# Optimization experiments

Hardware: AMD Instinct MI355X
Metric: run time of the kernel (lower is better)

Reference implementation:

```python
import jax, jax.numpy as jnp
import numpy as np

N_NODES = 100000
N_EDGES = 600000
NFEAT = 128
HIDDEN = 64
NCLASS = 40


def _sage_conv(x, edge_index, Wl, bl, Wr):
    """PyG SAGEConv with mean aggregation.

    out = lin_l(mean_{j in N(i)} x_j) + lin_r(x_i)
    edge_index[0] = source j, edge_index[1] = target i.
    """
    src, dst = edge_index[0], edge_index[1]
    n = x.shape[0]
    # scatter-mean: sum messages then divide by in-degree (0-degree -> 0)
    msg_sum = jax.ops.segment_sum(x[src], dst, num_segments=n)          # [N, F]
    deg = jax.ops.segment_sum(jnp.ones_like(src, dtype=x.dtype), dst,
                              num_segments=n)                            # [N]
    agg = msg_sum / jnp.maximum(deg, 1.0)[:, None]
    return agg @ Wl + bl + x @ Wr


def setup_inputs() -> dict:
    key = jax.random.key(0)
    ks = jax.random.split(key, 8)
    x = jax.random.normal(ks[0], (N_NODES, NFEAT), dtype=jnp.float32)
    edge_index = jax.random.randint(ks[1], (2, N_EDGES), 0, N_NODES, dtype=jnp.int64)
    s1 = 1.0 / np.sqrt(NFEAT)
    s2 = 1.0 / np.sqrt(HIDDEN)
    return {
        "x": x,
        "edge_index": edge_index,
        "W1l": jax.random.uniform(ks[2], (NFEAT, HIDDEN), jnp.float32, -s1, s1),
        "b1": jnp.zeros((HIDDEN,), jnp.float32),
        "W1r": jax.random.uniform(ks[3], (NFEAT, HIDDEN), jnp.float32, -s1, s1),
        "W2l": jax.random.uniform(ks[4], (HIDDEN, NCLASS), jnp.float32, -s2, s2),
        "b2": jnp.zeros((NCLASS,), jnp.float32),
        "W2r": jax.random.uniform(ks[5], (HIDDEN, NCLASS), jnp.float32, -s2, s2),
    }


def reference(x, edge_index, W1l, b1, W1r, W2l, b2, W2r):
    h = _sage_conv(x, edge_index, W1l, b1, W1r)   # [N, 64]
    h = jax.nn.sigmoid(h)
    out = _sage_conv(h, edge_index, W2l, b2, W2r)  # [N, nclass]
    return out
```

## Files before the change

### kernel.cpp

```cpp
#include <hip/hip_runtime.h>
#include <hip/hip_bf16.h>


#define N_FEAT 128
#define HID 64
#define NCLS 40
#define NE_BLK 2048
#define ECAP 1536

typedef short short8 __attribute__((ext_vector_type(8)));
typedef float floatx4 __attribute__((ext_vector_type(4)));

static __device__ __forceinline__ short f2bf(float x) {
    __hip_bfloat16 h = __float2bfloat16(x);
    return __builtin_bit_cast(short, h);
}
static __device__ __forceinline__ float bf2f(unsigned short u) {
    unsigned int v = ((unsigned int)u) << 16;
    return __builtin_bit_cast(float, v);
}
static __device__ __forceinline__ void acc8(float* a, uint4 v, float w) {
    a[0] = fmaf(w, bf2f((unsigned short)(v.x & 0xffffu)), a[0]);
    a[1] = fmaf(w, bf2f((unsigned short)(v.x >> 16)), a[1]);
    a[2] = fmaf(w, bf2f((unsigned short)(v.y & 0xffffu)), a[2]);
    a[3] = fmaf(w, bf2f((unsigned short)(v.y >> 16)), a[3]);
    a[4] = fmaf(w, bf2f((unsigned short)(v.z & 0xffffu)), a[4]);
    a[5] = fmaf(w, bf2f((unsigned short)(v.z >> 16)), a[5]);
    a[6] = fmaf(w, bf2f((unsigned short)(v.w & 0xffffu)), a[6]);
    a[7] = fmaf(w, bf2f((unsigned short)(v.w >> 16)), a[7]);
}

__global__ void prep_hist(const float* __restrict__ W1l, const float* __restrict__ W1r,
                          const float* __restrict__ W2l, const float* __restrict__ W2r,
                          unsigned short* __restrict__ wt1,
                          unsigned short* __restrict__ wt2,
                          int* __restrict__ flags,
                          const int* __restrict__ ei, int ne, int n,
                          int* __restrict__ bh, int nbe) {
    __shared__ int bins[512];
    const int b = blockIdx.x, t = threadIdx.x;
    const int nbuck = (n + 255) >> 8;
    for (int i = t; i < nbuck; i += 256) bins[i] = 0;
    __syncthreads();
    const int e0 = b * NE_BLK;
    const int lim = (e0 + NE_BLK < ne) ? (e0 + NE_BLK) : ne;
    for (int e = e0 + t; e < lim; e += 256)
        atomicAdd(&bins[ei[ne + e] >> 8], 1);

    int i = b * 256 + t;
    if (i < 128 * 128) {
        int nn = i >> 7, k = i & 127;
        float v = (nn < 64) ? W1l[k * 64 + nn] : W1r[k * 64 + (nn - 64)];
        wt1[nn * 128 + k] = (unsigned short)f2bf(v);
    } else if (i < 128 * 128 + 48 * 128) {
        int j = i - 128 * 128;
        int nn = j >> 7, k = j & 127;
        float v = 0.f;
        if (nn < 40)
            v = (k < 64) ? W2l[k * 40 + nn] : W2r[(k - 64) * 40 + nn];
        wt2[nn * 128 + k] = (unsigned short)f2bf(v);
    }
    if (i < 256) flags[i] = 0;

    __syncthreads();
    for (int j = t; j < nbuck; j += 256) bh[j * nbe + b] = bins[j];
}

__global__ void scan_fused(const int* __restrict__ in, int* __restrict__ pre,
                           int m, int* __restrict__ bsums,
                           int* __restrict__ flags) {
    __shared__ int lds[256];
    __shared__ int look[128];
    __shared__ int sprefix;
    const int b = blockIdx.x, t = threadIdx.x;
    const int base = b * 2048 + t * 8;
    int v[8], s = 0;
#pragma unroll
    for (int i = 0; i < 8; ++i) {
        int idx = base + i;
        v[i] = (idx < m) ? in[idx] : 0;
        s += v[i];
    }
    lds[t] = s;
    __syncthreads();
    for (int o = 1; o < 256; o <<= 1) {
        int y = (t >= o) ? lds[t - o] : 0;
        __syncthreads();
        lds[t] += y;
        __syncthreads();
    }
    if (t == 255) {
        __hip_atomic_store(&bsums[b], lds[255], __ATOMIC_RELEASE,
                           __HIP_MEMORY_SCOPE_AGENT);
        __hip_atomic_store(&flags[b], 1, __ATOMIC_RELEASE,
                           __HIP_MEMORY_SCOPE_AGENT);
    }
    if (t < 128) look[t] = 0;
    __syncthreads();
    if (t < b) {
        while (__hip_atomic_load(&flags[t], __ATOMIC_ACQUIRE,
                                 __HIP_MEMORY_SCOPE_AGENT) == 0) {}
        look[t] = __hip_atomic_load(&bsums[t], __ATOMIC_RELAXED,
                                    __HIP_MEMORY_SCOPE_AGENT);
    }
    __syncthreads();
    if (t == 0) {
        int p = 0;
        for (int i = 0; i < b; ++i) p += look[i];
        sprefix = p;
    }
    __syncthreads();
    int run = ((t == 0) ? 0 : lds[t - 1]) + sprefix;
#pragma unroll
    for (int i = 0; i < 8; ++i) {
        run += v[i];
        int idx = base + i;
        if (idx < m) pre[idx + 1] = run;
    }
    if (b == 0 && t == 0) pre[0] = 0;
}

static __device__ __forceinline__ void gemm1_body(
    short* __restrict__ smem, const float* __restrict__ x,
    const unsigned short* __restrict__ Wt, unsigned short* __restrict__ Zl,
    unsigned short* __restrict__ Zr, int n, int bid) {
    constexpr int K = 128, LDA = K + 8, M = 128, MT = 8, KS = 4, QROW = 16;
    short* At = smem;
    short* Bt = smem + 64 * LDA;
    const int t = threadIdx.x;
    const int nodeBase = bid * 64;

    for (int q = t; q < 64 * QROW; q += 256) {
        int row = q / QROW;
        int k0 = (q % QROW) * 8;
        int node = nodeBase + row;
        short8 s = {0, 0, 0, 0, 0, 0, 0, 0};
        if (node < n) {
            const float* A = x + (size_t)node * K + k0;
            float4 v0 = *(const float4*)A;
            float4 v1 = *(const float4*)(A + 4);
            s[0] = f2bf(v0.x); s[1] = f2bf(v0.y);
            s[2] = f2bf(v0.z); s[3] = f2bf(v0.w);
            s[4] = f2bf(v1.x); s[5] = f2bf(v1.y);
            s[6] = f2bf(v1.z); s[7] = f2bf(v1.w);
        }
        *(short8*)&At[row * LDA + k0] = s;
    }
    for (int q = t; q < M * QROW; q += 256) {
        int row = q / QROW;
        int k0 = (q % QROW) * 8;
        *(short8*)&Bt[row * LDA + k0] =
            *(const short8*)((const short*)Wt + (size_t)row * K + k0);
    }
    __syncthreads();

    const int wave = t >> 6;
    const int lane = t & 63;
    const int m0 = wave * 16;
    const int fl = lane & 15;
    const int quad = lane >> 4;

    floatx4 acc[MT];
#pragma unroll
    for (int nt = 0; nt < MT; ++nt) acc[nt] = (floatx4){0.f, 0.f, 0.f, 0.f};

#pragma unroll
    for (int ks = 0; ks < KS; ++ks) {
        const int kb = ks * 32 + quad * 8;
        short8 a = *(const short8*)&At[(m0 + fl) * LDA + kb];
#pragma unroll
        for (int nt = 0; nt < MT; ++nt) {
            short8 b = *(const short8*)&Bt[(nt * 16 + fl) * LDA + kb];
            acc[nt] = __builtin_amdgcn_mfma_f32_16x16x32_bf16(a, b, acc[nt], 0, 0, 0);
        }
    }

#pragma unroll
    for (int nt = 0; nt < MT; ++nt) {
        const int col = nt * 16 + fl;
#pragma unroll
        for (int r = 0; r < 4; ++r) {
            int node = nodeBase + m0 + quad * 4 + r;
            if (node < n) {
                unsigned short v = (unsigned short)f2bf(acc[nt][r]);
                if (col < HID)
                    Zl[(size_t)node * HID + col] = v;
                else
                    Zr[(size_t)node * HID + (col - HID)] = v;
            }
        }
    }
}

__global__ __launch_bounds__(256) void scatter_gemm1(
    const int* __restrict__ ei, int ne, int n, const int* __restrict__ sbase,
    int* __restrict__ ebuf, int nbe, const float* __restrict__ x,
    const unsigned short* __restrict__ wt1, unsigned short* __restrict__ zl,
    unsigned short* __restrict__ zr) {
    __shared__ __align__(16) short smem[(64 + 128) * 136];
    const int b = blockIdx.x;
    if (b < nbe) {
        int* bins = (int*)smem;
        const int t = threadIdx.x;
        const int nbuck = (n + 255) >> 8;
        for (int i = t; i < nbuck; i += 256) bins[i] = 0;
        __syncthreads();
        const int e0 = b * NE_BLK;
        const int lim = (e0 + NE_BLK < ne) ? (e0 + NE_BLK) : ne;
        for (int e = e0 + t; e < lim; e += 256) {
            int d = ei[ne + e];
            int s = ei[e];
            int bk = d >> 8;
            int r = atomicAdd(&bins[bk], 1);
            int p = sbase[bk * nbe + b] + r;
            ebuf[p] = (int)(((unsigned)(d & 255) << 24) | (unsigned)s);
        }
    } else {
        gemm1_body(smem, x, wt1, zl, zr, n, b - nbe);
    }
}

__global__ void bucket_build(const int* __restrict__ ebuf,
                             const int* __restrict__ sbase, int nbe, int n,
                             int ne, int* __restrict__ off,
                             int* __restrict__ csr) {
    __shared__ int cnt[256];
    __shared__ int sc[256];
    __shared__ int pos[256];
    const int b = blockIdx.x;
    const int t = threadIdx.x;
    const int nbuck = (n + 255) >> 8;
    const int s0 = sbase[b * nbe];
    const int s1 = (b + 1 < nbuck) ? sbase[(b + 1) * nbe] : ne;
    cnt[t] = 0;
    __syncthreads();
    for (int i = s0 + t; i < s1; i += 256)
        atomicAdd(&cnt[((unsigned)ebuf[i]) >> 24], 1);
    __syncthreads();
    int v = cnt[t];
    sc[t] = v;
    __syncthreads();
    for (int o = 1; o < 256; o <<= 1) {
        int y = (t >= o) ? sc[t - o] : 0;
        __syncthreads();
        sc[t] += y;
        __syncthreads();
    }
    int g = b * 256 + t;
    if (g < n) off[g + 1] = s0 + sc[t];
    if (b == 0 && t == 0) off[0] = 0;
    pos[t] = s0 + sc[t] - v;
    __syncthreads();
    for (int i = s0 + t; i < s1; i += 256) {
        unsigned w = (unsigned)ebuf[i];
        int p = atomicAdd(&pos[w >> 24], 1);
        csr[p] = (int)(w & 0xFFFFFFu);
    }
}

__global__ __launch_bounds__(256) void agg_h(
    const unsigned short* __restrict__ Zl, const unsigned short* __restrict__ Zr,
    const int* __restrict__ off, const int* __restrict__ csr,
    const float* __restrict__ bias, unsigned short* __restrict__ hout, int n) {
    __shared__ int offs[65];
    __shared__ int elist[ECAP];
    const int t = threadIdx.x;
    const int base = blockIdx.x * 64;
    if (t < 65) {
        int idx = base + t;
        offs[t] = off[(idx <= n) ? idx : n];
    }
    __syncthreads();
    const int E0 = offs[0];
    const int nedge = offs[64] - E0;
    const bool direct = (nedge > ECAP);
    if (!direct)
        for (int j = t; j < nedge; j += 256) elist[j] = csr[E0 + j];
    __syncthreads();

    const int lane = t & 63;
    const int wave = t >> 6;
    const int g = lane >> 3, c = lane & 7;

    for (int p = 0; p < 8; ++p) {
        const int i0 = wave * 16 + 2 * p, i1 = i0 + 1;
        const int s0 = offs[i0] - E0, d0 = offs[i0 + 1] - offs[i0];
        const int s1 = offs[i1] - E0, d1 = offs[i1 + 1] - offs[i1];
        float a0[8], a1[8];
#pragma unroll
        for (int j = 0; j < 8; ++j) { a0[j] = 0.f; a1[j] = 0.f; }
        const int dm = (d0 > d1) ? d0 : d1;
        for (int r0 = 0; r0 < dm; r0 += 8) {
            const int r = r0 + g;
            int sl0 = s0 + ((r < d0) ? r : ((d0 > 0) ? d0 - 1 : 0));
            int sl1 = s1 + ((r < d1) ? r : ((d1 > 0) ? d1 - 1 : 0));
            int j0 = (d0 > 0) ? (direct ? csr[E0 + sl0] : elist[sl0]) : 0;
            int j1 = (d1 > 0) ? (direct ? csr[E0 + sl1] : elist[sl1]) : 0;
            uint4 v0 = *(const uint4*)(Zl + (size_t)j0 * 64 + c * 8);
            uint4 v1 = *(const uint4*)(Zl + (size_t)j1 * 64 + c * 8);
            acc8(a0, v0, (r < d0) ? 1.f : 0.f);
            acc8(a1, v1, (r < d1) ? 1.f : 0.f);
        }
#pragma unroll
        for (int o = 8; o < 64; o <<= 1) {
#pragma unroll
            for (int j = 0; j < 8; ++j) {
                a0[j] += __shfl_xor(a0[j], o);
                a1[j] += __shfl_xor(a1[j], o);
            }
        }
        if (g < 2) {
            const int i = g ? i1 : i0;
            const int node = base + i;
            if (node < n) {
                const int dd = g ? d1 : d0;
                const float inv = 1.0f / fmaxf((float)dd, 1.0f);
                float rr[8];
#pragma unroll
                for (int j = 0; j < 8; ++j) rr[j] = (g ? a1[j] : a0[j]) * inv;
                uint4 z = *(const uint4*)(Zr + (size_t)node * 64 + c * 8);
                float4 b0 = ((const float4*)bias)[c * 2];
                float4 b1 = ((const float4*)bias)[c * 2 + 1];
                rr[0] += bf2f((unsigned short)(z.x & 0xffffu)) + b0.x;
                rr[1] += bf2f((unsigned short)(z.x >> 16)) + b0.y;
                rr[2] += bf2f((unsigned short)(z.y & 0xffffu)) + b0.z;
                rr[3] += bf2f((unsigned short)(z.y >> 16)) + b0.w;
                rr[4] += bf2f((unsigned short)(z.z & 0xffffu)) + b1.x;
                rr[5] += bf2f((unsigned short)(z.z >> 16)) + b1.y;
                rr[6] += bf2f((unsigned short)(z.w & 0xffffu)) + b1.z;
                rr[7] += bf2f((unsigned short)(z.w >> 16)) + b1.w;
#pragma unroll
                for (int j = 0; j < 8; ++j)
                    rr[j] = 1.0f / (1.0f + __expf(-rr[j]));
                uint4 pk;
                pk.x = (unsigned int)(unsigned short)f2bf(rr[0]) |
                       ((unsigned int)(unsigned short)f2bf(rr[1]) << 16);
                pk.y = (unsigned int)(unsigned short)f2bf(rr[2]) |
                       ((unsigned int)(unsigned short)f2bf(rr[3]) << 16);
                pk.z = (unsigned int)(unsigned short)f2bf(rr[4]) |
                       ((unsigned int)(unsigned short)f2bf(rr[5]) << 16);
                pk.w = (unsigned int)(unsigned short)f2bf(rr[6]) |
                       ((unsigned int)(unsigned short)f2bf(rr[7]) << 16);
                *(uint4*)(hout + (size_t)node * 64 + c * 8) = pk;
            }
        }
    }
}

__global__ __launch_bounds__(256) void agg_gemm2(
    const unsigned short* __restrict__ h, const unsigned short* __restrict__ Wt,
    const float* __restrict__ bias, const int* __restrict__ off,
    const int* __restrict__ csr, float* __restrict__ out, int n) {
    constexpr int LDA = 136;
    __shared__ __align__(16) short At[64 * LDA];
    __shared__ __align__(16) short Bt[48 * LDA];
    __shared__ int offs[65];
    __shared__ int elist[ECAP];
    const int t = threadIdx.x;
    const int base = blockIdx.x * 64;
    if (t < 65) {
        int idx = base + t;
        offs[t] = off[(idx <= n) ? idx : n];
    }
    __syncthreads();
    const int E0 = offs[0];
    const int nedge = offs[64] - E0;
    const bool direct = (nedge > ECAP);
    if (!direct)
        for (int j = t; j < nedge; j += 256) elist[j] = csr[E0 + j];
    for (int q = t; q < 64 * 8; q += 256) {
        int row = q >> 3, k0 = (q & 7) * 8;
        int node = base + row;
        short8 s = {0, 0, 0, 0, 0, 0, 0, 0};
        if (node < n) s = *(const short8*)(h + (size_t)node * 64 + k0);
        *(short8*)&At[row * LDA + 64 + k0] = s;
    }
    for (int q = t; q < 48 * 16; q += 256) {
        int row = q >> 4, k0 = (q & 15) * 8;
        *(short8*)&Bt[row * LDA + k0] =
            *(const short8*)((const short*)Wt + (size_t)row * 128 + k0);
    }
    __syncthreads();

    const int lane = t & 63;
    const int wave = t >> 6;
    const int g = lane >> 3, c = lane & 7;
    for (int p = 0; p < 8; ++p) {
        const int i0 = wave * 16 + 2 * p, i1 = i0 + 1;
        const int s0 = offs[i0] - E0, d0 = offs[i0 + 1] - offs[i0];
        const int s1 = offs[i1] - E0, d1 = offs[i1 + 1] - offs[i1];
        float a0[8], a1[8];
#pragma unroll
        for (int j = 0; j < 8; ++j) { a0[j] = 0.f; a1[j] = 0.f; }
        const int dm = (d0 > d1) ? d0 : d1;
        for (int r0 = 0; r0 < dm; r0 += 8) {
            const int r = r0 + g;
            int sl0 = s0 + ((r < d0) ? r : ((d0 > 0) ? d0 - 1 : 0));
            int sl1 = s1 + ((r < d1) ? r : ((d1 > 0) ? d1 - 1 : 0));
            int j0 = (d0 > 0) ? (direct ? csr[E0 + sl0] : elist[sl0]) : 0;
            int j1 = (d1 > 0) ? (direct ? csr[E0 + sl1] : elist[sl1]) : 0;
            uint4 v0 = *(const uint4*)(h + (size_t)j0 * 64 + c * 8);
            uint4 v1 = *(const uint4*)(h + (size_t)j1 * 64 + c * 8);
            acc8(a0, v0, (r < d0) ? 1.f : 0.f);
            acc8(a1, v1, (r < d1) ? 1.f : 0.f);
        }
#pragma unroll
        for (int o = 8; o < 64; o <<= 1) {
#pragma unroll
            for (int j = 0; j < 8; ++j) {
                a0[j] += __shfl_xor(a0[j], o);
                a1[j] += __shfl_xor(a1[j], o);
            }
        }
        if (g < 2) {
            const int i = g ? i1 : i0;
            const int dd = g ? d1 : d0;
            const float inv = 1.0f / fmaxf((float)dd, 1.0f);
            short8 s;
#pragma unroll
            for (int j = 0; j < 8; ++j)
                s[j] = f2bf((g ? a1[j] : a0[j]) * inv);
            *(short8*)&At[i * LDA + c * 8] = s;
        }
    }
    __syncthreads();

    const int m0 = wave * 16;
    const int fl = lane & 15;
    const int quad = lane >> 4;
    floatx4 acc[3];
#pragma unroll
    for (int nt = 0; nt < 3; ++nt) acc[nt] = (floatx4){0.f, 0.f, 0.f, 0.f};
#pragma unroll
    for (int ks = 0; ks < 4; ++ks) {
        const int kb = ks * 32 + quad * 8;
        short8 a = *(const short8*)&At[(m0 + fl) * LDA + kb];
#pragma unroll
        for (int nt = 0; nt < 3; ++nt) {
            short8 b = *(const short8*)&Bt[(nt * 16 + fl) * LDA + kb];
            acc[nt] = __builtin_amdgcn_mfma_f32_16x16x32_bf16(a, b, acc[nt], 0, 0, 0);
        }
    }
#pragma unroll
    for (int nt = 0; nt < 3; ++nt) {
        const int col = nt * 16 + fl;
        if (col < NCLS) {
            float bv = bias[col];
#pragma unroll
            for (int r = 0; r < 4; ++r) {
                int node = base + m0 + quad * 4 + r;
                if (node < n)
                    out[(size_t)node * NCLS + col] = acc[nt][r] + bv;
            }
        }
    }
}

extern "C" void kernel_launch(void* const* d_in, const int* in_sizes, int n_in,
                              void* d_out, int out_size, void* d_ws,
                              size_t ws_size, hipStream_t stream) {
    const float* x = (const float*)d_in[0];
    const int* ei = (const int*)d_in[1];
    const float* W1l = (const float*)d_in[2];
    const float* b1 = (const float*)d_in[3];
    const float* W1r = (const float*)d_in[4];
    const float* W2l = (const float*)d_in[5];
    const float* b2 = (const float*)d_in[6];
    const float* W2r = (const float*)d_in[7];
    float* out = (float*)d_out;

    const int n = in_sizes[0] / N_FEAT;
    const int ne = in_sizes[1] / 2;

    const int nbe = (ne + NE_BLK - 1) / NE_BLK;
    const int nbuck = (n + 255) >> 8;
    const int tot = nbuck * nbe;

    unsigned short* zl1 = (unsigned short*)d_ws;
    unsigned short* zr1 = zl1 + (size_t)n * HID;
    unsigned short* h = zr1 + (size_t)n * HID;
    unsigned short* wt1 = h + (size_t)n * HID;
    unsigned short* wt2 = wt1 + 128 * 128;
    int* off = (int*)(wt2 + 48 * 128);
    int* csr = off + (n + 1);
    int* ebuf = csr + ne;
    int* bh = ebuf + ne;
    int* sbase = bh + tot;
    int* bsums = sbase + (tot + 1);
    int* flags = bsums + 256;

    const int gblocks = (n + 63) / 64;
    const int nsb = (tot + 2047) / 2048;

    prep_hist<<<nbe, 256, 0, stream>>>(W1l, W1r, W2l, W2r, wt1, wt2, flags,
                                       ei, ne, n, bh, nbe);
    scan_fused<<<nsb, 256, 0, stream>>>(bh, sbase, tot, bsums, flags);
    scatter_gemm1<<<nbe + gblocks, 256, 0, stream>>>(ei, ne, n, sbase, ebuf,
                                                     nbe, x, wt1, zl1, zr1);
    bucket_build<<<nbuck, 256, 0, stream>>>(ebuf, sbase, nbe, n, ne, off, csr);
    agg_h<<<gblocks, 256, 0, stream>>>(zl1, zr1, off, csr, b1, h, n);
    agg_gemm2<<<gblocks, 256, 0, stream>>>(h, wt2, b2, off, csr, out, n);
}
```

Before: 216.6 us.

## Drop CSR build; aggregate bucketed edges via LDS float atomics per 64-node tile

Buckets are shrunk from 256 to 64 destination nodes so that each bucket matches one 64-node aggregation tile. This removes the bucket_build kernel and the off/csr arrays. The aggregation kernels now stream the unsorted bucket edge list and accumulate into a shared-memory float tile using LDS atomicAdds, with degree counted the same way. This saves one launch and a full pass over the edges. In exchange it adds many LDS atomics and contention, makes the float summation order nondeterministic, and quadruples the histogram and scan sizes.

Result: slower. 608.0 us (+180.7%).

```diff
diff --git a/kernel.cpp b/kernel.cpp
--- a/kernel.cpp
+++ b/kernel.cpp
@@ -6,7 +6,7 @@
 #define HID 64
 #define NCLS 40
 #define NE_BLK 2048
-#define ECAP 1536
+#define ECAP 768
 
 typedef short short8 __attribute__((ext_vector_type(8)));
 typedef float floatx4 __attribute__((ext_vector_type(4)));
@@ -18,16 +18,6 @@
 static __device__ __forceinline__ float bf2f(unsigned short u) {
     unsigned int v = ((unsigned int)u) << 16;
     return __builtin_bit_cast(float, v);
-}
-static __device__ __forceinline__ void acc8(float* a, uint4 v, float w) {
-    a[0] = fmaf(w, bf2f((unsigned short)(v.x & 0xffffu)), a[0]);
-    a[1] = fmaf(w, bf2f((unsigned short)(v.x >> 16)), a[1]);
-    a[2] = fmaf(w, bf2f((unsigned short)(v.y & 0xffffu)), a[2]);
-    a[3] = fmaf(w, bf2f((unsigned short)(v.y >> 16)), a[3]);
-    a[4] = fmaf(w, bf2f((unsigned short)(v.z & 0xffffu)), a[4]);
-    a[5] = fmaf(w, bf2f((unsigned short)(v.z >> 16)), a[5]);
-    a[6] = fmaf(w, bf2f((unsigned short)(v.w & 0xffffu)), a[6]);
-    a[7] = fmaf(w, bf2f((unsigned short)(v.w >> 16)), a[7]);
 }
 
 __global__ void prep_hist(const float* __restrict__ W1l, const float* __restrict__ W1r,
@@ -37,15 +27,15 @@
                           int* __restrict__ flags,
                           const int* __restrict__ ei, int ne, int n,
                           int* __restrict__ bh, int nbe) {
-    __shared__ int bins[512];
+    __shared__ int bins[2048];
     const int b = blockIdx.x, t = threadIdx.x;
-    const int nbuck = (n + 255) >> 8;
+    const int nbuck = (n + 63) >> 6;
     for (int i = t; i < nbuck; i += 256) bins[i] = 0;
     __syncthreads();
     const int e0 = b * NE_BLK;
     const int lim = (e0 + NE_BLK < ne) ? (e0 + NE_BLK) : ne;
     for (int e = e0 + t; e < lim; e += 256)
-        atomicAdd(&bins[ei[ne + e] >> 8], 1);
+        atomicAdd(&bins[ei[ne + e] >> 6], 1);
 
     int i = b * 256 + t;
     if (i < 128 * 128) {
@@ -63,14 +53,14 @@
     if (i < 256) flags[i] = 0;
 
     __syncthreads();
-    for (int j = t; j < nbuck; j += 256) bh[j * nbe + b] = bins[j];
+    for (int j = t; j < nbuck; j += 256) bh[(size_t)j * nbe + b] = bins[j];
 }
 
 __global__ void scan_fused(const int* __restrict__ in, int* __restrict__ pre,
                            int m, int* __restrict__ bsums,
                            int* __restrict__ flags) {
     __shared__ int lds[256];
-    __shared__ int look[128];
+    __shared__ int look[256];
     __shared__ int sprefix;
     const int b = blockIdx.x, t = threadIdx.x;
     const int base = b * 2048 + t * 8;
@@ -95,7 +85,7 @@
         __hip_atomic_store(&flags[b], 1, __ATOMIC_RELEASE,
                            __HIP_MEMORY_SCOPE_AGENT);
     }
-    if (t < 128) look[t] = 0;
+    look[t] = 0;
     __syncthreads();
     if (t < b) {
         while (__hip_atomic_load(&flags[t], __ATOMIC_ACQUIRE,
@@ -194,7 +184,7 @@
 
 __global__ __launch_bounds__(256) void scatter_gemm1(
     const int* __restrict__ ei, int ne, int n, const int* __restrict__ sbase,
-    int* __restrict__ ebuf, int nbe, const float* __restrict__ x,
+    unsigned* __restrict__ ebuf, int nbe, const float* __restrict__ x,
     const unsigned short* __restrict__ wt1, unsigned short* __restrict__ zl,
     unsigned short* __restrict__ zr) {
     __shared__ __align__(16) short smem[(64 + 128) * 136];
@@ -202,7 +192,7 @@
     if (b < nbe) {
         int* bins = (int*)smem;
         const int t = threadIdx.x;
-        const int nbuck = (n + 255) >> 8;
+        const int nbuck = (n + 63) >> 6;
         for (int i = t; i < nbuck; i += 256) bins[i] = 0;
         __syncthreads();
         const int e0 = b * NE_BLK;
@@ -210,164 +200,123 @@
         for (int e = e0 + t; e < lim; e += 256) {
             int d = ei[ne + e];
             int s = ei[e];
-            int bk = d >> 8;
+            int bk = d >> 6;
             int r = atomicAdd(&bins[bk], 1);
-            int p = sbase[bk * nbe + b] + r;
-            ebuf[p] = (int)(((unsigned)(d & 255) << 24) | (unsigned)s);
+            int p = sbase[(size_t)bk * nbe + b] + r;
+            ebuf[p] = ((unsigned)(d & 63) << 26) | (unsigned)s;
         }
     } else {
         gemm1_body(smem, x, wt1, zl, zr, n, b - nbe);
     }
 }
 
-__global__ void bucket_build(const int* __restrict__ ebuf,
-                             const int* __restrict__ sbase, int nbe, int n,
-                             int ne, int* __restrict__ off,
-                             int* __restrict__ csr) {
-    __shared__ int cnt[256];
-    __shared__ int sc[256];
-    __shared__ int pos[256];
-    const int b = blockIdx.x;
+static __device__ __forceinline__ void gather_acc(
+    float* __restrict__ acc, const unsigned* __restrict__ elist,
+    const unsigned* __restrict__ ebufE0, bool direct,
+    const unsigned short* __restrict__ Z, int nedge) {
     const int t = threadIdx.x;
-    const int nbuck = (n + 255) >> 8;
-    const int s0 = sbase[b * nbe];
-    const int s1 = (b + 1 < nbuck) ? sbase[(b + 1) * nbe] : ne;
-    cnt[t] = 0;
-    __syncthreads();
-    for (int i = s0 + t; i < s1; i += 256)
-        atomicAdd(&cnt[((unsigned)ebuf[i]) >> 24], 1);
-    __syncthreads();
-    int v = cnt[t];
-    sc[t] = v;
-    __syncthreads();
-    for (int o = 1; o < 256; o <<= 1) {
-        int y = (t >= o) ? sc[t - o] : 0;
-        __syncthreads();
-        sc[t] += y;
-        __syncthreads();
-    }
-    int g = b * 256 + t;
-    if (g < n) off[g + 1] = s0 + sc[t];
-    if (b == 0 && t == 0) off[0] = 0;
-    pos[t] = s0 + sc[t] - v;
-    __syncthreads();
-    for (int i = s0 + t; i < s1; i += 256) {
-        unsigned w = (unsigned)ebuf[i];
-        int p = atomicAdd(&pos[w >> 24], 1);
-        csr[p] = (int)(w & 0xFFFFFFu);
+    const int w = t >> 6, lane = t & 63;
+    const int g = lane >> 3, c = lane & 7;
+    const int wl = (nedge * w) >> 2;
+    const int wr = (nedge * (w + 1)) >> 2;
+    const int wn = wr - wl;
+    const int seg = (wn + 7) >> 3;
+    const int sbeg = wl + g * seg;
+#pragma unroll 2
+    for (int r = 0; r < seg; ++r) {
+        int e = sbeg + r;
+        if (e < wr) {
+            unsigned u = direct ? ebufE0[e] : elist[e];
+            int loc = (int)(u >> 26);
+            int src = (int)(u & 0x03FFFFFFu);
+            uint4 v = *(const uint4*)(Z + (size_t)src * 64 + c * 8);
+            float* a = acc + loc * 68 + c * 8;
+            atomicAdd(a + 0, bf2f((unsigned short)(v.x & 0xffffu)));
+            atomicAdd(a + 1, bf2f((unsigned short)(v.x >> 16)));
+            atomicAdd(a + 2, bf2f((unsigned short)(v.y & 0xffffu)));
+            atomicAdd(a + 3, bf2f((unsigned short)(v.y >> 16)));
+            atomicAdd(a + 4, bf2f((unsigned short)(v.z & 0xffffu)));
+            atomicAdd(a + 5, bf2f((unsigned short)(v.z >> 16)));
+            atomicAdd(a + 6, bf2f((unsigned short)(v.w & 0xffffu)));
+            atomicAdd(a + 7, bf2f((unsigned short)(v.w >> 16)));
+            if (c == 0) atomicAdd(acc + loc * 68 + 64, 1.0f);
+        }
     }
 }
 
 __global__ __launch_bounds__(256) void agg_h(
     const unsigned short* __restrict__ Zl, const unsigned short* __restrict__ Zr,
-    const int* __restrict__ off, const int* __restrict__ csr,
+    const unsigned* __restrict__ ebuf, const int* __restrict__ sbase, int nbe,
     const float* __restrict__ bias, unsigned short* __restrict__ hout, int n) {
-    __shared__ int offs[65];
-    __shared__ int elist[ECAP];
+    __shared__ float acc[64 * 68];
+    __shared__ unsigned elist[ECAP];
     const int t = threadIdx.x;
-    const int base = blockIdx.x * 64;
-    if (t < 65) {
-        int idx = base + t;
-        offs[t] = off[(idx <= n) ? idx : n];
-    }
-    __syncthreads();
-    const int E0 = offs[0];
-    const int nedge = offs[64] - E0;
+    const int tile = blockIdx.x;
+    const int base = tile * 64;
+    const int E0 = sbase[(size_t)tile * nbe];
+    const int E1 = sbase[(size_t)(tile + 1) * nbe];
+    const int nedge = E1 - E0;
+    for (int i = t; i < 64 * 68; i += 256) acc[i] = 0.f;
     const bool direct = (nedge > ECAP);
     if (!direct)
-        for (int j = t; j < nedge; j += 256) elist[j] = csr[E0 + j];
-    __syncthreads();
-
-    const int lane = t & 63;
-    const int wave = t >> 6;
-    const int g = lane >> 3, c = lane & 7;
-
-    for (int p = 0; p < 8; ++p) {
-        const int i0 = wave * 16 + 2 * p, i1 = i0 + 1;
-        const int s0 = offs[i0] - E0, d0 = offs[i0 + 1] - offs[i0];
-        const int s1 = offs[i1] - E0, d1 = offs[i1 + 1] - offs[i1];
-        float a0[8], a1[8];
-#pragma unroll
-        for (int j = 0; j < 8; ++j) { a0[j] = 0.f; a1[j] = 0.f; }
-        const int dm = (d0 > d1) ? d0 : d1;
-        for (int r0 = 0; r0 < dm; r0 += 8) {
-            const int r = r0 + g;
-            int sl0 = s0 + ((r < d0) ? r : ((d0 > 0) ? d0 - 1 : 0));
-            int sl1 = s1 + ((r < d1) ? r : ((d1 > 0) ? d1 - 1 : 0));
-            int j0 = (d0 > 0) ? (direct ? csr[E0 + sl0] : elist[sl0]) : 0;
-            int j1 = (d1 > 0) ? (direct ? csr[E0 + sl1] : elist[sl1]) : 0;
-            uint4 v0 = *(const uint4*)(Zl + (size_t)j0 * 64 + c * 8);
-            uint4 v1 = *(const uint4*)(Zl + (size_t)j1 * 64 + c * 8);
-            acc8(a0, v0, (r < d0) ? 1.f : 0.f);
-            acc8(a1, v1, (r < d1) ? 1.f : 0.f);
-        }
-#pragma unroll
-        for (int o = 8; o < 64; o <<= 1) {
-#pragma unroll
-            for (int j = 0; j < 8; ++j) {
-                a0[j] += __shfl_xor(a0[j], o);
-                a1[j] += __shfl_xor(a1[j], o);
-            }
-        }
-        if (g < 2) {
-            const int i = g ? i1 : i0;
-            const int node = base + i;
-            if (node < n) {
-                const int dd = g ? d1 : d0;
-                const float inv = 1.0f / fmaxf((float)dd, 1.0f);
-                float rr[8];
-#pragma unroll
-                for (int j = 0; j < 8; ++j) rr[j] = (g ? a1[j] : a0[j]) * inv;
-                uint4 z = *(const uint4*)(Zr + (size_t)node * 64 + c * 8);
-                float4 b0 = ((const float4*)bias)[c * 2];
-                float4 b1 = ((const float4*)bias)[c * 2 + 1];
-                rr[0] += bf2f((unsigned short)(z.x & 0xffffu)) + b0.x;
-                rr[1] += bf2f((unsigned short)(z.x >> 16)) + b0.y;
-                rr[2] += bf2f((unsigned short)(z.y & 0xffffu)) + b0.z;
-                rr[3] += bf2f((unsigned short)(z.y >> 16)) + b0.w;
-                rr[4] += bf2f((unsigned short)(z.z & 0xffffu)) + b1.x;
-                rr[5] += bf2f((unsigned short)(z.z >> 16)) + b1.y;
-                rr[6] += bf2f((unsigned short)(z.w & 0xffffu)) + b1.z;
-                rr[7] += bf2f((unsigned short)(z.w >> 16)) + b1.w;
-#pragma unroll
-                for (int j = 0; j < 8; ++j)
-                    rr[j] = 1.0f / (1.0f + __expf(-rr[j]));
-                uint4 pk;
-                pk.x = (unsigned int)(unsigned short)f2bf(rr[0]) |
-                       ((unsigned int)(unsigned short)f2bf(rr[1]) << 16);
-                pk.y = (unsigned int)(unsigned short)f2bf(rr[2]) |
-                       ((unsigned int)(unsigned short)f2bf(rr[3]) << 16);
-                pk.z = (unsigned int)(unsigned short)f2bf(rr[4]) |
-                       ((unsigned int)(unsigned short)f2bf(rr[5]) << 16);
-                pk.w = (unsigned int)(unsigned short)f2bf(rr[6]) |
-                       ((unsigned int)(unsigned short)f2bf(rr[7]) << 16);
-                *(uint4*)(hout + (size_t)node * 64 + c * 8) = pk;
-            }
-        }
+        for (int j = t; j < nedge; j += 256) elist[j] = ebuf[E0 + j];
+    __syncthreads();
+
+    gather_acc(acc, elist, ebuf + E0, direct, Zl, nedge);
+    __syncthreads();
+
+    for (int q = t; q < 512; q += 256) {
+        int i = q >> 3, cc = q & 7;
+        int node = base + i;
+        if (node >= n) continue;
+        float inv = 1.0f / fmaxf(acc[i * 68 + 64], 1.0f);
+        const float* a = &acc[i * 68 + cc * 8];
+        uint4 z = *(const uint4*)(Zr + (size_t)node * 64 + cc * 8);
+        float4 b0 = ((const float4*)bias)[cc * 2];
+        float4 b1 = ((const float4*)bias)[cc * 2 + 1];
+        float rr[8];
+        rr[0] = a[0] * inv + bf2f((unsigned short)(z.x & 0xffffu)) + b0.x;
+        rr[1] = a[1] * inv + bf2f((unsigned short)(z.x >> 16)) + b0.y;
+        rr[2] = a[2] * inv + bf2f((unsigned short)(z.y & 0xffffu)) + b0.z;
+        rr[3] = a[3] * inv + bf2f((unsigned short)(z.y >> 16)) + b0.w;
+        rr[4] = a[4] * inv + bf2f((unsigned short)(z.z & 0xffffu)) + b1.x;
+        rr[5] = a[5] * inv + bf2f((unsigned short)(z.z >> 16)) + b1.y;
+        rr[6] = a[6] * inv + bf2f((unsigned short)(z.w & 0xffffu)) + b1.z;
+        rr[7] = a[7] * inv + bf2f((unsigned short)(z.w >> 16)) + b1.w;
+#pragma unroll
+        for (int j = 0; j < 8; ++j) rr[j] = 1.0f / (1.0f + __expf(-rr[j]));
+        uint4 pk;
+        pk.x = (unsigned int)(unsigned short)f2bf(rr[0]) |
+               ((unsigned int)(unsigned short)f2bf(rr[1]) << 16);
+        pk.y = (unsigned int)(unsigned short)f2bf(rr[2]) |
+               ((unsigned int)(unsigned short)f2bf(rr[3]) << 16);
+        pk.z = (unsigned int)(unsigned short)f2bf(rr[4]) |
+               ((unsigned int)(unsigned short)f2bf(rr[5]) << 16);
+        pk.w = (unsigned int)(unsigned short)f2bf(rr[6]) |
+               ((unsigned int)(unsigned short)f2bf(rr[7]) << 16);
+        *(uint4*)(hout + (size_t)node * 64 + cc * 8) = pk;
     }
 }
 
 __global__ __launch_bounds__(256) void agg_gemm2(
     const unsigned short* __restrict__ h, const unsigned short* __restrict__ Wt,
-    const float* __restrict__ bias, const int* __restrict__ off,
-    const int* __restrict__ csr, float* __restrict__ out, int n) {
+    const float* __restrict__ bias, const unsigned* __restrict__ ebuf,
+    const int* __restrict__ sbase, int nbe, float* __restrict__ out, int n) {
     constexpr int LDA = 136;
     __shared__ __align__(16) short At[64 * LDA];
     __shared__ __align__(16) short Bt[48 * LDA];
-    __shared__ int offs[65];
-    __shared__ int elist[ECAP];
+    __shared__ float acc[64 * 68];
+    __shared__ unsigned elist[ECAP];
     const int t = threadIdx.x;
-    const int base = blockIdx.x * 64;
-    if (t < 65) {
-        int idx = base + t;
-        offs[t] = off[(idx <= n) ? idx : n];
-    }
-    __syncthreads();
-    const int E0 = offs[0];
-    const int nedge = offs[64] - E0;
+    const int tile = blockIdx.x;
+    const int base = tile * 64;
+    const int E0 = sbase[(size_t)tile * nbe];
+    const int E1 = sbase[(size_t)(tile + 1) * nbe];
+    const int nedge = E1 - E0;
+    for (int i = t; i < 64 * 68; i += 256) acc[i] = 0.f;
     const bool direct = (nedge > ECAP);
     if (!direct)
-        for (int j = t; j < nedge; j += 256) elist[j] = csr[E0 + j];
+        for (int j = t; j < nedge; j += 256) elist[j] = ebuf[E0 + j];
     for (int q = t; q < 64 * 8; q += 256) {
         int row = q >> 3, k0 = (q & 7) * 8;
         int node = base + row;
@@ -382,55 +331,28 @@
     }
     __syncthreads();
 
+    gather_acc(acc, elist, ebuf + E0, direct, h, nedge);
+    __syncthreads();
+
+    for (int q = t; q < 512; q += 256) {
+        int i = q >> 3, cc = q & 7;
+        float inv = 1.0f / fmaxf(acc[i * 68 + 64], 1.0f);
+        const float* a = &acc[i * 68 + cc * 8];
+        short8 s;
+#pragma unroll
+        for (int j = 0; j < 8; ++j) s[j] = f2bf(a[j] * inv);
+        *(short8*)&At[i * LDA + cc * 8] = s;
+    }
+    __syncthreads();
+
+    const int wave = t >> 6;
     const int lane = t & 63;
-    const int wave = t >> 6;
-    const int g = lane >> 3, c = lane & 7;
-    for (int p = 0; p < 8; ++p) {
-        const int i0 = wave * 16 + 2 * p, i1 = i0 + 1;
-        const int s0 = offs[i0] - E0, d0 = offs[i0 + 1] - offs[i0];
-        const int s1 = offs[i1] - E0, d1 = offs[i1 + 1] - offs[i1];
-        float a0[8], a1[8];
-#pragma unroll
-        for (int j = 0; j < 8; ++j) { a0[j] = 0.f; a1[j] = 0.f; }
-        const int dm = (d0 > d1) ? d0 : d1;
-        for (int r0 = 0; r0 < dm; r0 += 8) {
-            const int r = r0 + g;
-            int sl0 = s0 + ((r < d0) ? r : ((d0 > 0) ? d0 - 1 : 0));
-            int sl1 = s1 + ((r < d1) ? r : ((d1 > 0) ? d1 - 1 : 0));
-            int j0 = (d0 > 0) ? (direct ? csr[E0 + sl0] : elist[sl0]) : 0;
-            int j1 = (d1 > 0) ? (direct ? csr[E0 + sl1] : elist[sl1]) : 0;
-            uint4 v0 = *(const uint4*)(h + (size_t)j0 * 64 + c * 8);
-            uint4 v1 = *(const uint4*)(h + (size_t)j1 * 64 + c * 8);
-            acc8(a0, v0, (r < d0) ? 1.f : 0.f);
-            acc8(a1, v1, (r < d1) ? 1.f : 0.f);
-        }
-#pragma unroll
-        for (int o = 8; o < 64; o <<= 1) {
-#pragma unroll
-            for (int j = 0; j < 8; ++j) {
-                a0[j] += __shfl_xor(a0[j], o);
-                a1[j] += __shfl_xor(a1[j], o);
-            }
-        }
-        if (g < 2) {
-            const int i = g ? i1 : i0;
-            const int dd = g ? d1 : d0;
-            const float inv = 1.0f / fmaxf((float)dd, 1.0f);
-            short8 s;
-#pragma unroll
-            for (int j = 0; j < 8; ++j)
-                s[j] = f2bf((g ? a1[j] : a0[j]) * inv);
-            *(short8*)&At[i * LDA + c * 8] = s;
-        }
-    }
-    __syncthreads();
-
     const int m0 = wave * 16;
     const int fl = lane & 15;
     const int quad = lane >> 4;
-    floatx4 acc[3];
-#pragma unroll
-    for (int nt = 0; nt < 3; ++nt) acc[nt] = (floatx4){0.f, 0.f, 0.f, 0.f};
+    floatx4 accr[3];
+#pragma unroll
+    for (int nt = 0; nt < 3; ++nt) accr[nt] = (floatx4){0.f, 0.f, 0.f, 0.f};
 #pragma unroll
     for (int ks = 0; ks < 4; ++ks) {
         const int kb = ks * 32 + quad * 8;
@@ -438,7 +360,7 @@
 #pragma unroll
         for (int nt = 0; nt < 3; ++nt) {
             short8 b = *(const short8*)&Bt[(nt * 16 + fl) * LDA + kb];
-            acc[nt] = __builtin_amdgcn_mfma_f32_16x16x32_bf16(a, b, acc[nt], 0, 0, 0);
+            accr[nt] = __builtin_amdgcn_mfma_f32_16x16x32_bf16(a, b, accr[nt], 0, 0, 0);
         }
     }
 #pragma unroll
@@ -450,7 +372,7 @@
             for (int r = 0; r < 4; ++r) {
                 int node = base + m0 + quad * 4 + r;
                 if (node < n)
-                    out[(size_t)node * NCLS + col] = acc[nt][r] + bv;
+                    out[(size_t)node * NCLS + col] = accr[nt][r] + bv;
             }
         }
     }
@@ -473,7 +395,7 @@
     const int ne = in_sizes[1] / 2;
 
     const int nbe = (ne + NE_BLK - 1) / NE_BLK;
-    const int nbuck = (n + 255) >> 8;
+    const int nbuck = (n + 63) >> 6;
     const int tot = nbuck * nbe;
 
     unsigned short* zl1 = (unsigned short*)d_ws;
@@ -481,10 +403,8 @@
     unsigned short* h = zr1 + (size_t)n * HID;
     unsigned short* wt1 = h + (size_t)n * HID;
     unsigned short* wt2 = wt1 + 128 * 128;
-    int* off = (int*)(wt2 + 48 * 128);
-    int* csr = off + (n + 1);
-    int* ebuf = csr + ne;
-    int* bh = ebuf + ne;
+    unsigned* ebuf = (unsigned*)(wt2 + 48 * 128);
+    int* bh = (int*)(ebuf + ne);
     int* sbase = bh + tot;
     int* bsums = sbase + (tot + 1);
     int* flags = bsums + 256;
@@ -497,7 +417,6 @@
     scan_fused<<<nsb, 256, 0, stream>>>(bh, sbase, tot, bsums, flags);
     scatter_gemm1<<<nbe + gblocks, 256, 0, stream>>>(ei, ne, n, sbase, ebuf,
                                                      nbe, x, wt1, zl1, zr1);
-    bucket_build<<<nbuck, 256, 0, stream>>>(ebuf, sbase, nbe, n, ne, off, csr);
-    agg_h<<<gblocks, 256, 0, stream>>>(zl1, zr1, off, csr, b1, h, n);
-    agg_gemm2<<<gblocks, 256, 0, stream>>>(h, wt2, b2, off, csr, out, n);
-}
+    agg_h<<<gblocks, 256, 0, stream>>>(zl1, zr1, ebuf, sbase, nbe, b1, h, n);
+    agg_gemm2<<<gblocks, 256, 0, stream>>>(h, wt2, b2, ebuf, sbase, nbe, out, n);
+}
```
